# Kernel tuning notes

Hardware: AMD Instinct MI355X
Metric: run time of the kernel (lower is better)

## Reference

```python
import jax, jax.numpy as jnp
import numpy as np

S = 192          # spatial_size
N = 100000       # active input sites
CIN, M, M2, NCLS = 3, 32, 64, 50
EPS = 1e-4       # scn BatchNorm eps
OFFS = np.array([[dx, dy, dz] for dx in (-1, 0, 1) for dy in (-1, 0, 1) for dz in (-1, 0, 1)], dtype=np.int64)


def _build_nbr(coords, size):
    # coords: [n,3] unique int64. Returns [n,27] int32 neighbor index (-1 = inactive site),
    # i.e. the submanifold-convolution rulebook built via sorted-key hashing.
    n = coords.shape[0]
    keys = (coords[:, 0] * size + coords[:, 1]) * size + coords[:, 2]
    order = np.argsort(keys)
    sk = keys[order]
    nbr = np.full((n, 27), -1, dtype=np.int32)
    for k, off in enumerate(OFFS):
        nc = coords + off
        ok = np.all((nc >= 0) & (nc < size), axis=1)
        qk = (nc[:, 0] * size + nc[:, 1]) * size + nc[:, 2]
        pos = np.searchsorted(sk, qk).clip(0, n - 1)
        hit = ok & (sk[pos] == qk)
        nbr[hit, k] = order[pos[hit]].astype(np.int32)
    return nbr


def setup_inputs() -> dict:
    rng = np.random.default_rng(0)
    raw = rng.integers(0, S, size=(130000, 3), dtype=np.int64)
    keys = (raw[:, 0] * S + raw[:, 1]) * S + raw[:, 2]
    _, first = np.unique(keys, return_index=True)
    coords = raw[np.sort(first)][:N]          # N unique active voxels
    nbr_fine = _build_nbr(coords, S)
    # stride-2 / filter-2 downsample rulebook: coarse sites = unique(coords // 2)
    S2 = S // 2
    cc = coords // 2
    ckeys = (cc[:, 0] * S2 + cc[:, 1]) * S2 + cc[:, 2]
    uk, parent = np.unique(ckeys, return_inverse=True)
    ccoords = np.column_stack((uk // (S2 * S2), (uk // S2) % S2, uk % S2))
    nbr_coarse = _build_nbr(ccoords, S2)
    offset_id = (coords[:, 0] % 2) * 4 + (coords[:, 1] % 2) * 2 + coords[:, 2] % 2
    key = jax.random.key(0)
    ks = jax.random.split(key, 8)
    def w(k, shape, fan):
        return jax.random.normal(k, shape, jnp.float32) * (1.0 / np.sqrt(fan))
    return dict(
        coords=jnp.asarray(coords, jnp.int32),
        features=jax.random.normal(ks[0], (N, CIN), jnp.float32),
        nbr_fine=jnp.asarray(nbr_fine),
        nbr_coarse=jnp.asarray(nbr_coarse),
        parent=jnp.asarray(parent.astype(np.int32)),
        offset_id=jnp.asarray(offset_id.astype(np.int32)),
        num_coarse=int(uk.shape[0]),
        w_in=w(ks[1], (27, CIN, M), 27 * CIN),
        w_b1=w(ks[2], (27, M, M), 27 * M),
        w_down=w(ks[3], (8, M, M2), 8 * M),
        w_b2=w(ks[4], (27, M2, M2), 27 * M2),
        w_up=w(ks[5], (8, M2, M), 8 * M2),
        w_b3=w(ks[6], (27, 2 * M, M), 27 * 2 * M),
        g1=jnp.ones((M,)), b1=jnp.zeros((M,)),
        gd=jnp.ones((M,)), bd=jnp.zeros((M,)),
        g2=jnp.ones((M2,)), b2=jnp.zeros((M2,)),
        gu=jnp.ones((M2,)), bu=jnp.zeros((M2,)),
        g3=jnp.ones((2 * M,)), b3=jnp.zeros((2 * M,)),
        go=jnp.ones((M,)), bo=jnp.zeros((M,)),
        w_lin=w(ks[7], (M, NCLS), M),
        b_lin=jnp.zeros((NCLS,)),
    )


def _subm_conv(f, nbr, W):
    # f: [n,Cin], nbr: [n,27] (-1 = inactive), W: [27,Cin,Cout]
    mask = nbr >= 0
    g = f[jnp.where(mask, nbr, 0)] * mask[..., None]  # [n,27,Cin]
    return jnp.einsum('nkc,kcd->nd', g, W)


def _bnrelu(f, gamma, beta):
    mu = f.mean(0)
    var = ((f - mu) ** 2).mean(0)
    return jax.nn.relu((f - mu) * (gamma / jnp.sqrt(var + EPS)) + beta)


def _down(f, parent, off_id, W, nc):
    # strided 2^3 conv: out[parent] += W[offset(child)] @ f[child]
    out = jnp.zeros((nc, W.shape[2]), f.dtype)
    for o in range(8):
        sel = (off_id == o)[:, None].astype(f.dtype)
        out = out + jax.ops.segment_sum((f * sel) @ W[o], parent, num_segments=nc)
    return out


def _up(g, parent, off_id, W):
    # 2^3 deconv back to fine sites
    gp = g[parent]
    out = jnp.zeros((gp.shape[0], W.shape[2]), g.dtype)
    for o in range(8):
        out = out + (off_id == o)[:, None].astype(g.dtype) * (gp @ W[o])
    return out


def reference(coords, features, nbr_fine, nbr_coarse, parent, offset_id, num_coarse,
              w_in, w_b1, w_down, w_b2, w_up, w_b3,
              g1, b1, gd, bd, g2, b2, gu, bu, g3, b3, go, bo, w_lin, b_lin):
    # InputLayer (coords unique -> identity) + SubmanifoldConvolution(CIN->M)
    f = _subm_conv(features, nbr_fine, w_in)
    # UNet level 0 block (pre-activation)
    f = _subm_conv(_bnrelu(f, g1, b1), nbr_fine, w_b1)
    skip = f
    # downsample: BNReLU + Convolution(M->M2, 2, 2)
    g = _down(_bnrelu(f, gd, bd), parent, offset_id, w_down, num_coarse)
    # UNet level 1 block
    g = _subm_conv(_bnrelu(g, g2, b2), nbr_coarse, w_b2)
    # upsample: BNReLU + Deconvolution(M2->M, 2, 2)
    u = _up(_bnrelu(g, gu, bu), parent, offset_id, w_up)
    # JoinTable + block (2M -> M)
    f = jnp.concatenate([skip, u], axis=1)
    f = _subm_conv(_bnrelu(f, g3, b3), nbr_fine, w_b3)
    # top-level BatchNormReLU(M) + OutputLayer + Linear head
    f = _bnrelu(f, go, bo)
    return f @ w_lin + b_lin
```

## Files before the change

### kernel.cpp

```cpp
#include <hip/hip_runtime.h>

#define EPS_BN 1e-4f
constexpr int BLK = 256;
constexpr int ECAPF = 256;
constexpr int ECAPC = 640;

__global__ __launch_bounds__(64) void build_subm_k(
    const int* __restrict__ nbr, int n, int ecap,
    int* __restrict__ seg, int* __restrict__ ent) {
  int T = blockIdx.x, r = threadIdx.x;
  int i = T * 64 + r;
  bool valid = i < n;
  int base = 0;
  if (r == 0) seg[T * 28] = 0;
#pragma unroll 1
  for (int k = 0; k < 27; ++k) {
    int j = valid ? nbr[(size_t)i * 27 + k] : -1;
    bool act = j >= 0;
    unsigned long long mb = __ballot(act);
    int pre = __popcll(mb & ((1ull << r) - 1));
    if (act && base + pre < ecap)
      ent[(size_t)T * ecap + base + pre] = (r << 25) | j;
    base += __popcll(mb);
    if (r == 0) seg[T * 28 + k + 1] = base;
  }
}

__global__ __launch_bounds__(BLK) void child_scatter_k(
    const int* __restrict__ parent, const int* __restrict__ offid, int n,
    int* __restrict__ ccnt, int* __restrict__ cent) {
  int i = blockIdx.x * BLK + threadIdx.x;
  if (i >= n) return;
  int p = parent[i];
  int slot = atomicAdd(&ccnt[p], 1);
  cent[p * 8 + slot] = i | (offid[i] << 25);
}

__global__ __launch_bounds__(64) void build_down_k(
    const int* __restrict__ ccnt, const int* __restrict__ cent, int nc,
    int* __restrict__ segd, int* __restrict__ entd) {
  int T = blockIdx.x, r = threadIdx.x;
  int p = T * 64 + r;
  bool valid = p < nc;
  int cn = valid ? ccnt[p] : 0;
  int e[8];
#pragma unroll
  for (int s = 0; s < 8; ++s) e[s] = s < cn ? cent[p * 8 + s] : -1;
  int base = 0;
  if (r == 0) segd[T * 9] = 0;
#pragma unroll 1
  for (int oo = 0; oo < 8; ++oo) {
#pragma unroll
    for (int s = 0; s < 8; ++s) {
      bool act = e[s] >= 0 && (e[s] >> 25) == oo;
      unsigned long long mb = __ballot(act);
      int pre = __popcll(mb & ((1ull << r) - 1));
      if (act) entd[(size_t)T * 512 + base + pre] = (r << 25) | (e[s] & 0x1FFFFFF);
      base += __popcll(mb);
    }
    if (r == 0) segd[T * 9 + oo + 1] = base;
  }
}

__global__ __launch_bounds__(64) void build_up_k(
    const int* __restrict__ parent, const int* __restrict__ offid, int n,
    int* __restrict__ segu, int* __restrict__ entu) {
  int T = blockIdx.x, r = threadIdx.x;
  int i = T * 64 + r;
  bool valid = i < n;
  int o = valid ? offid[i] : -1;
  int pa = valid ? parent[i] : 0;
  int base = 0;
  if (r == 0) segu[T * 9] = 0;
#pragma unroll 1
  for (int oo = 0; oo < 8; ++oo) {
    bool act = o == oo;
    unsigned long long mb = __ballot(act);
    int pre = __popcll(mb & ((1ull << r) - 1));
    if (act) entu[(size_t)T * 64 + base + pre] = (r << 25) | pa;
    base += __popcll(mb);
    if (r == 0) segu[T * 9 + oo + 1] = base;
  }
}

template <int CI, int CO, int KT, bool BN, bool CAT>
__global__ __launch_bounds__(BLK) void tconv_k(
    const float* __restrict__ inA, const float* __restrict__ inB,
    const int* __restrict__ seg, const int* __restrict__ ent, int ecap,
    const float* __restrict__ stA, const float* __restrict__ stB,
    const float* __restrict__ W, float* __restrict__ out, int n) {
  constexpr int GO = CO / 16;
  constexpr int XP = CI + 4;
  constexpr int AP = CO + 4;
  __shared__ float lw[CI * CO];
  __shared__ float lx[64 * XP];
  __shared__ float lacc[64 * AP];
  int t = threadIdx.x;
  int T = blockIdx.x;
  const int* segT = seg + T * (KT + 1);
  const int* entT = ent + (size_t)T * ecap;

  for (int idx = t; idx < 64 * AP; idx += BLK) lacc[idx] = 0.f;

#pragma unroll 1
  for (int k = 0; k < KT; ++k) {
    int e0 = segT[k], e1 = segT[k + 1];
    int m = e1 - e0;
    if (m == 0) continue;
    const float4* wsrc = reinterpret_cast<const float4*>(W + (size_t)k * CI * CO);
    for (int idx = t; idx < CI * CO / 4; idx += BLK)
      reinterpret_cast<float4*>(lw)[idx] = wsrc[idx];
    for (int idx = t; idx < m * (CI / 4); idx += BLK) {
      int p = idx / (CI / 4), c4 = idx - p * (CI / 4);
      int j = entT[e0 + p] & 0x1FFFFFF;
      int cb = c4 * 4;
      float4 x;
      const float* st;
      int cc;
      if constexpr (CAT) {
        if (cb < CI / 2) { x = *reinterpret_cast<const float4*>(inA + (size_t)j * (CI / 2) + cb); st = stA; cc = cb; }
        else             { x = *reinterpret_cast<const float4*>(inB + (size_t)j * (CI / 2) + cb - CI / 2); st = stB; cc = cb - CI / 2; }
      } else {
        x = *reinterpret_cast<const float4*>(inA + (size_t)j * CI + cb); st = stA; cc = cb;
      }
      float v[4] = {x.x, x.y, x.z, x.w};
      if constexpr (BN) {
        constexpr int SH = CAT ? CI / 2 : CI;
#pragma unroll
        for (int q = 0; q < 4; ++q) {
          float y = fmaf(v[q], st[cc + q], st[SH + cc + q]);
          v[q] = y > 0.f ? y : 0.f;
        }
      }
      *reinterpret_cast<float4*>(&lx[p * XP + cb]) = make_float4(v[0], v[1], v[2], v[3]);
    }
    __syncthreads();
    int s = t >> 4, g = (t & 15) * GO;
#pragma unroll 1
    for (int p0 = 0; p0 < m; p0 += 16) {
      int p = p0 + s;
      if (p < m) {
        int r = entT[e0 + p] >> 25;
        float acc[GO];
#pragma unroll
        for (int b = 0; b < GO; ++b) acc[b] = 0.f;
#pragma unroll
        for (int c4 = 0; c4 < CI / 4; ++c4) {
          float4 xq = *reinterpret_cast<const float4*>(&lx[p * XP + c4 * 4]);
          float xs[4] = {xq.x, xq.y, xq.z, xq.w};
#pragma unroll
          for (int q = 0; q < 4; ++q) {
            const float* wr = &lw[(c4 * 4 + q) * CO + g];
            if constexpr (GO == 4) {
              float4 wv = *reinterpret_cast<const float4*>(wr);
              acc[0] = fmaf(xs[q], wv.x, acc[0]);
              acc[1] = fmaf(xs[q], wv.y, acc[1]);
              acc[2] = fmaf(xs[q], wv.z, acc[2]);
              acc[3] = fmaf(xs[q], wv.w, acc[3]);
            } else {
              float2 wv = *reinterpret_cast<const float2*>(wr);
              acc[0] = fmaf(xs[q], wv.x, acc[0]);
              acc[1] = fmaf(xs[q], wv.y, acc[1]);
            }
          }
        }
        float* ap = &lacc[r * AP + g];
        if constexpr (GO == 4) {
          float4 old = *reinterpret_cast<float4*>(ap);
          *reinterpret_cast<float4*>(ap) =
              make_float4(old.x + acc[0], old.y + acc[1], old.z + acc[2], old.w + acc[3]);
        } else {
          float2 old = *reinterpret_cast<float2*>(ap);
          *reinterpret_cast<float2*>(ap) = make_float2(old.x + acc[0], old.y + acc[1]);
        }
      }
    }
    __syncthreads();
  }
  __syncthreads();
  for (int idx = t; idx < 64 * (CO / 4); idx += BLK) {
    int r = idx / (CO / 4), c4 = idx - r * (CO / 4);
    int row = T * 64 + r;
    if (row < n)
      *reinterpret_cast<float4*>(out + (size_t)row * CO + c4 * 4) =
          *reinterpret_cast<const float4*>(&lacc[r * AP + c4 * 4]);
  }
}

__global__ __launch_bounds__(BLK) void conv_in_k(
    const float* __restrict__ feat, const int* __restrict__ nbr,
    const float* __restrict__ W, float* __restrict__ out, int n) {
  int i = blockIdx.x * BLK + threadIdx.x;
  if (i >= n) return;
  float acc[32];
#pragma unroll
  for (int c = 0; c < 32; ++c) acc[c] = 0.f;
  const int* nr = nbr + (size_t)i * 27;
#pragma unroll 1
  for (int k = 0; k < 27; ++k) {
    int j = nr[k];
    if (j < 0) continue;
    float x0 = feat[j * 3 + 0], x1 = feat[j * 3 + 1], x2 = feat[j * 3 + 2];
    const float* w0 = W + k * 96;
#pragma unroll
    for (int co = 0; co < 8; ++co) {
      float4 a = *reinterpret_cast<const float4*>(w0 + co * 4);
      float4 b = *reinterpret_cast<const float4*>(w0 + 32 + co * 4);
      float4 cc = *reinterpret_cast<const float4*>(w0 + 64 + co * 4);
      acc[4*co+0] = fmaf(x0, a.x, fmaf(x1, b.x, fmaf(x2, cc.x, acc[4*co+0])));
      acc[4*co+1] = fmaf(x0, a.y, fmaf(x1, b.y, fmaf(x2, cc.y, acc[4*co+1])));
      acc[4*co+2] = fmaf(x0, a.z, fmaf(x1, b.z, fmaf(x2, cc.z, acc[4*co+2])));
      acc[4*co+3] = fmaf(x0, a.w, fmaf(x1, b.w, fmaf(x2, cc.w, acc[4*co+3])));
    }
  }
  float* o = out + (size_t)i * 32;
#pragma unroll
  for (int co = 0; co < 8; ++co)
    *reinterpret_cast<float4*>(o + co * 4) = make_float4(acc[4*co], acc[4*co+1], acc[4*co+2], acc[4*co+3]);
}

template <int C>
__global__ __launch_bounds__(BLK) void stats_k(
    const float* __restrict__ f, int n, float* __restrict__ sums) {
  constexpr int G = BLK / C;
  int c = threadIdx.x % C;
  int g = threadIdx.x / C;
  float s = 0.f, ss = 0.f;
  for (int r = blockIdx.x * G + g; r < n; r += gridDim.x * G) {
    float x = f[(size_t)r * C + c];
    s += x;
    ss += x * x;
  }
  __shared__ float ls[BLK], lss[BLK];
  ls[threadIdx.x] = s;
  lss[threadIdx.x] = ss;
  __syncthreads();
  if (threadIdx.x < C) {
    float ts = 0.f, tss = 0.f;
#pragma unroll
    for (int q = 0; q < G; ++q) { ts += ls[q * C + c]; tss += lss[q * C + c]; }
    atomicAdd(&sums[c], ts);
    atomicAdd(&sums[C + c], tss);
  }
}

__global__ void finalize_k(const float* __restrict__ sums,
                           const float* __restrict__ gamma,
                           const float* __restrict__ beta, float inv_n,
                           float* __restrict__ st, int C) {
  int c = threadIdx.x;
  if (c >= C) return;
  float mu = sums[c] * inv_n;
  float var = sums[C + c] * inv_n - mu * mu;
  float sc = gamma[c] / sqrtf(var + EPS_BN);
  st[c] = sc;
  st[C + c] = beta[c] - mu * sc;
}

__global__ __launch_bounds__(BLK) void head_k(
    const float* __restrict__ fin, const float* __restrict__ st,
    const float* __restrict__ Wl, const float* __restrict__ bl,
    float* __restrict__ out, int n) {
  __shared__ float lw[32 * 50];
  __shared__ float lb[52];
  for (int idx = threadIdx.x; idx < 1600; idx += BLK) lw[idx] = Wl[idx];
  if (threadIdx.x < 50) lb[threadIdx.x] = bl[threadIdx.x];
  __syncthreads();
  int i = blockIdx.x * BLK + threadIdx.x;
  if (i >= n) return;
  float x[32];
  const float* fj = fin + (size_t)i * 32;
#pragma unroll
  for (int c4 = 0; c4 < 8; ++c4) {
    float4 v = *reinterpret_cast<const float4*>(fj + c4 * 4);
    float vs[4] = {v.x, v.y, v.z, v.w};
#pragma unroll
    for (int q = 0; q < 4; ++q) {
      int c = c4 * 4 + q;
      float y = fmaf(vs[q], st[c], st[32 + c]);
      x[c] = y > 0.f ? y : 0.f;
    }
  }
  float acc[50];
#pragma unroll
  for (int co = 0; co < 50; ++co) acc[co] = lb[co];
#pragma unroll 4
  for (int c = 0; c < 32; ++c) {
#pragma unroll
    for (int co = 0; co < 50; ++co) acc[co] = fmaf(x[c], lw[c * 50 + co], acc[co]);
  }
  float* o = out + (size_t)i * 50;
#pragma unroll
  for (int co = 0; co < 25; ++co)
    *reinterpret_cast<float2*>(o + co * 2) = make_float2(acc[co * 2], acc[co * 2 + 1]);
}

extern "C" void kernel_launch(void* const* d_in, const int* in_sizes, int n_in,
                              void* d_out, int out_size, void* d_ws, size_t ws_size,
                              hipStream_t stream) {
  const float* feat   = (const float*)d_in[1];
  const int*   nbrF   = (const int*)d_in[2];
  const int*   nbrC   = (const int*)d_in[3];
  const int*   parent = (const int*)d_in[4];
  const int*   offid  = (const int*)d_in[5];
  const float* w_in   = (const float*)d_in[7];
  const float* w_b1   = (const float*)d_in[8];
  const float* w_down = (const float*)d_in[9];
  const float* w_b2   = (const float*)d_in[10];
  const float* w_up   = (const float*)d_in[11];
  const float* w_b3   = (const float*)d_in[12];
  const float* g1 = (const float*)d_in[13], *b1 = (const float*)d_in[14];
  const float* gd = (const float*)d_in[15], *bd = (const float*)d_in[16];
  const float* g2 = (const float*)d_in[17], *b2 = (const float*)d_in[18];
  const float* gu = (const float*)d_in[19], *bu = (const float*)d_in[20];
  const float* g3 = (const float*)d_in[21], *b3 = (const float*)d_in[22];
  const float* go = (const float*)d_in[23], *bo = (const float*)d_in[24];
  const float* w_lin = (const float*)d_in[25];
  const float* b_lin = (const float*)d_in[26];
  float* out = (float*)d_out;

  int N  = in_sizes[4];
  int NC = in_sizes[3] / 27;
  int ntF = (N + 63) / 64, ntC = (NC + 63) / 64;

  size_t szF = (size_t)N * 32;
  size_t szG = (size_t)NC * 64;
  size_t SA = szG > szF ? szG : szF;

  float* ws  = (float*)d_ws;
  float* A   = ws;
  float* f2  = A + SA;
  float* gCu = f2 + szF;
  float* sums1 = gCu + szG;
  float* sumsD = sums1 + 64;
  float* sums2 = sumsD + 64;
  float* sumsU = sums2 + 128;
  float* sums4 = sumsU + 128;
  float* sums5 = sums4 + 64;
  float* st1  = sums5 + 64;
  float* stD  = st1 + 64;
  float* st3a = stD + 64;
  float* st2  = st3a + 64;
  float* stU  = st2 + 128;
  float* st3b = stU + 128;
  float* stO  = st3b + 64;
  int* segF = (int*)(stO + 64);
  int* entF = segF + (size_t)ntF * 28;
  int* segC = entF + (size_t)ntF * ECAPF;
  int* entC = segC + (size_t)ntC * 28;
  int* ccnt = entC + (size_t)ntC * ECAPC;
  int* cent = ccnt + NC;
  int* segD = cent + (size_t)NC * 8;
  int* entD = segD + (size_t)ntC * 9;
  int* segU = entD + (size_t)ntC * 512;
  int* entU = segU + (size_t)ntF * 9;

  hipMemsetAsync(sums1, 0, 512 * sizeof(float), stream);
  hipMemsetAsync(ccnt, 0, (size_t)NC * sizeof(int), stream);

  int gridN = (N + BLK - 1) / BLK;
  int sgrid = 304;
  float invN = 1.f / (float)N, invC = 1.f / (float)NC;

  build_subm_k<<<ntF, 64, 0, stream>>>(nbrF, N, ECAPF, segF, entF);
  build_subm_k<<<ntC, 64, 0, stream>>>(nbrC, NC, ECAPC, segC, entC);
  child_scatter_k<<<gridN, BLK, 0, stream>>>(parent, offid, N, ccnt, cent);
  build_down_k<<<ntC, 64, 0, stream>>>(ccnt, cent, NC, segD, entD);
  build_up_k<<<ntF, 64, 0, stream>>>(parent, offid, N, segU, entU);

  conv_in_k<<<gridN, BLK, 0, stream>>>(feat, nbrF, w_in, A, N);
  stats_k<32><<<sgrid, BLK, 0, stream>>>(A, N, sums1);
  finalize_k<<<1, 64, 0, stream>>>(sums1, g1, b1, invN, st1, 32);

  tconv_k<32, 32, 27, true, false><<<ntF, BLK, 0, stream>>>(
      A, nullptr, segF, entF, ECAPF, st1, nullptr, w_b1, f2, N);
  stats_k<32><<<sgrid, BLK, 0, stream>>>(f2, N, sumsD);
  finalize_k<<<1, 64, 0, stream>>>(sumsD, gd, bd, invN, stD, 32);
  finalize_k<<<1, 64, 0, stream>>>(sumsD, g3, b3, invN, st3a, 32);

  tconv_k<32, 64, 8, true, false><<<ntC, BLK, 0, stream>>>(
      f2, nullptr, segD, entD, 512, stD, nullptr, w_down, gCu, NC);
  stats_k<64><<<sgrid, BLK, 0, stream>>>(gCu, NC, sums2);
  finalize_k<<<1, 64, 0, stream>>>(sums2, g2, b2, invC, st2, 64);

  tconv_k<64, 64, 27, true, false><<<ntC, BLK, 0, stream>>>(
      gCu, nullptr, segC, entC, ECAPC, st2, nullptr, w_b2, A, NC);
  stats_k<64><<<sgrid, BLK, 0, stream>>>(A, NC, sumsU);
  finalize_k<<<1, 64, 0, stream>>>(sumsU, gu, bu, invC, stU, 64);

  tconv_k<64, 32, 8, true, false><<<ntF, BLK, 0, stream>>>(
      A, nullptr, segU, entU, 64, stU, nullptr, w_up, gCu, N);
  stats_k<32><<<sgrid, BLK, 0, stream>>>(gCu, N, sums4);
  finalize_k<<<1, 64, 0, stream>>>(sums4, g3 + 32, b3 + 32, invN, st3b, 32);

  tconv_k<64, 32, 27, true, true><<<ntF, BLK, 0, stream>>>(
      f2, gCu, segF, entF, ECAPF, st3a, st3b, w_b3, A, N);
  stats_k<32><<<sgrid, BLK, 0, stream>>>(A, N, sums5);
  finalize_k<<<1, 64, 0, stream>>>(sums5, go, bo, invN, stO, 32);

  head_k<<<gridN, BLK, 0, stream>>>(A, stO, w_lin, b_lin, out, N);
}
```

Measured before the change: 566.8 us.

## Fuse BN stats into convs, double-buffer weights, drop LDS gather staging

BatchNorm statistics are now accumulated inside each convolution epilogue with atomics, and the finalize step is folded into the consumer kernel's prologue. This removes the separate stats and finalize launches and their extra passes over the feature maps. The tconv kernel drops the shared-memory gather buffer and reads neighbor features straight from global memory, applying BN+ReLU per element. It also double-buffers per-offset weights through registers and skips empty offsets. The fine and upsample rulebook builders are merged and the entry caps raised, trading more global gathers per output group and atomic contention for fewer launches and syncs.

```diff
diff --git a/kernel.cpp b/kernel.cpp
--- a/kernel.cpp
+++ b/kernel.cpp
@@ -2,12 +2,14 @@
 
 #define EPS_BN 1e-4f
 constexpr int BLK = 256;
-constexpr int ECAPF = 256;
-constexpr int ECAPC = 640;
-
-__global__ __launch_bounds__(64) void build_subm_k(
-    const int* __restrict__ nbr, int n, int ecap,
-    int* __restrict__ seg, int* __restrict__ ent) {
+constexpr int ECAPF = 512;
+constexpr int ECAPC = 1024;
+
+__global__ __launch_bounds__(64) void build_fine_k(
+    const int* __restrict__ nbr, const int* __restrict__ parent,
+    const int* __restrict__ offid, int n, int ecap,
+    int* __restrict__ seg, int* __restrict__ ent,
+    int* __restrict__ segu, int* __restrict__ entu) {
   int T = blockIdx.x, r = threadIdx.x;
   int i = T * 64 + r;
   bool valid = i < n;
@@ -24,6 +26,40 @@
     base += __popcll(mb);
     if (r == 0) seg[T * 28 + k + 1] = base;
   }
+  int o = valid ? offid[i] : -1;
+  int pa = valid ? parent[i] : 0;
+  base = 0;
+  if (r == 0) segu[T * 9] = 0;
+#pragma unroll 1
+  for (int oo = 0; oo < 8; ++oo) {
+    bool act = o == oo;
+    unsigned long long mb = __ballot(act);
+    int pre = __popcll(mb & ((1ull << r) - 1));
+    if (act) entu[(size_t)T * 64 + base + pre] = (r << 25) | pa;
+    base += __popcll(mb);
+    if (r == 0) segu[T * 9 + oo + 1] = base;
+  }
+}
+
+__global__ __launch_bounds__(64) void build_subm_k(
+    const int* __restrict__ nbr, int n, int ecap,
+    int* __restrict__ seg, int* __restrict__ ent) {
+  int T = blockIdx.x, r = threadIdx.x;
+  int i = T * 64 + r;
+  bool valid = i < n;
+  int base = 0;
+  if (r == 0) seg[T * 28] = 0;
+#pragma unroll 1
+  for (int k = 0; k < 27; ++k) {
+    int j = valid ? nbr[(size_t)i * 27 + k] : -1;
+    bool act = j >= 0;
+    unsigned long long mb = __ballot(act);
+    int pre = __popcll(mb & ((1ull << r) - 1));
+    if (act && base + pre < ecap)
+      ent[(size_t)T * ecap + base + pre] = (r << 25) | j;
+    base += __popcll(mb);
+    if (r == 0) seg[T * 28 + k + 1] = base;
+  }
 }
 
 __global__ __launch_bounds__(BLK) void child_scatter_k(
@@ -62,122 +98,148 @@
   }
 }
 
-__global__ __launch_bounds__(64) void build_up_k(
-    const int* __restrict__ parent, const int* __restrict__ offid, int n,
-    int* __restrict__ segu, int* __restrict__ entu) {
-  int T = blockIdx.x, r = threadIdx.x;
-  int i = T * 64 + r;
-  bool valid = i < n;
-  int o = valid ? offid[i] : -1;
-  int pa = valid ? parent[i] : 0;
-  int base = 0;
-  if (r == 0) segu[T * 9] = 0;
-#pragma unroll 1
-  for (int oo = 0; oo < 8; ++oo) {
-    bool act = o == oo;
-    unsigned long long mb = __ballot(act);
-    int pre = __popcll(mb & ((1ull << r) - 1));
-    if (act) entu[(size_t)T * 64 + base + pre] = (r << 25) | pa;
-    base += __popcll(mb);
-    if (r == 0) segu[T * 9 + oo + 1] = base;
-  }
-}
-
-template <int CI, int CO, int KT, bool BN, bool CAT>
+template <int CI, int CO, int KT, bool CAT>
 __global__ __launch_bounds__(BLK) void tconv_k(
     const float* __restrict__ inA, const float* __restrict__ inB,
     const int* __restrict__ seg, const int* __restrict__ ent, int ecap,
-    const float* __restrict__ stA, const float* __restrict__ stB,
-    const float* __restrict__ W, float* __restrict__ out, int n) {
+    const float* __restrict__ sumsA, const float* __restrict__ gA,
+    const float* __restrict__ bA, float invA,
+    const float* __restrict__ sumsB, const float* __restrict__ gB,
+    const float* __restrict__ bB, float invB,
+    const float* __restrict__ W, float* __restrict__ out, int n,
+    float* __restrict__ osums) {
   constexpr int GO = CO / 16;
-  constexpr int XP = CI + 4;
   constexpr int AP = CO + 4;
-  __shared__ float lw[CI * CO];
-  __shared__ float lx[64 * XP];
+  constexpr int WSZ = CI * CO;
+  constexpr int WL = WSZ / 4 / BLK;
+  __shared__ float lw[2][WSZ];
   __shared__ float lacc[64 * AP];
+  __shared__ float lst[2 * CI];
   int t = threadIdx.x;
   int T = blockIdx.x;
+
+  if constexpr (CAT) {
+    if (t < CI / 2) {
+      float mu = sumsA[t] * invA, var = sumsA[CI / 2 + t] * invA - mu * mu;
+      float sc = gA[t] / sqrtf(var + EPS_BN);
+      lst[t] = sc; lst[CI + t] = bA[t] - mu * sc;
+    } else if (t < CI) {
+      int c = t - CI / 2;
+      float mu = sumsB[c] * invB, var = sumsB[CI / 2 + c] * invB - mu * mu;
+      float sc = gB[c] / sqrtf(var + EPS_BN);
+      lst[t] = sc; lst[CI + t] = bB[c] - mu * sc;
+    }
+  } else {
+    if (t < CI) {
+      float mu = sumsA[t] * invA, var = sumsA[CI + t] * invA - mu * mu;
+      float sc = gA[t] / sqrtf(var + EPS_BN);
+      lst[t] = sc; lst[CI + t] = bA[t] - mu * sc;
+    }
+  }
+  for (int idx = t; idx < 64 * AP; idx += BLK) lacc[idx] = 0.f;
+
   const int* segT = seg + T * (KT + 1);
   const int* entT = ent + (size_t)T * ecap;
 
-  for (int idx = t; idx < 64 * AP; idx += BLK) lacc[idx] = 0.f;
-
-#pragma unroll 1
-  for (int k = 0; k < KT; ++k) {
-    int e0 = segT[k], e1 = segT[k + 1];
-    int m = e1 - e0;
-    if (m == 0) continue;
-    const float4* wsrc = reinterpret_cast<const float4*>(W + (size_t)k * CI * CO);
-    for (int idx = t; idx < CI * CO / 4; idx += BLK)
-      reinterpret_cast<float4*>(lw)[idx] = wsrc[idx];
-    for (int idx = t; idx < m * (CI / 4); idx += BLK) {
-      int p = idx / (CI / 4), c4 = idx - p * (CI / 4);
-      int j = entT[e0 + p] & 0x1FFFFFF;
-      int cb = c4 * 4;
-      float4 x;
-      const float* st;
-      int cc;
-      if constexpr (CAT) {
-        if (cb < CI / 2) { x = *reinterpret_cast<const float4*>(inA + (size_t)j * (CI / 2) + cb); st = stA; cc = cb; }
-        else             { x = *reinterpret_cast<const float4*>(inB + (size_t)j * (CI / 2) + cb - CI / 2); st = stB; cc = cb - CI / 2; }
-      } else {
-        x = *reinterpret_cast<const float4*>(inA + (size_t)j * CI + cb); st = stA; cc = cb;
+  int k = KT, e0 = 0, e1 = 0;
+  {
+    int prev = segT[0];
+#pragma unroll 1
+    for (int q = 0; q < KT; ++q) {
+      int cur = segT[q + 1];
+      if (cur > prev) { k = q; e0 = prev; e1 = cur; break; }
+      prev = cur;
+    }
+  }
+  if (k < KT) {
+    const float4* wsrc = reinterpret_cast<const float4*>(W + (size_t)k * WSZ);
+#pragma unroll
+    for (int q = 0; q < WL; ++q)
+      reinterpret_cast<float4*>(lw[0])[t + q * BLK] = wsrc[t + q * BLK];
+  }
+  __syncthreads();
+
+  int par = 0;
+#pragma unroll 1
+  while (k < KT) {
+    int kn = KT, f0 = 0, f1 = 0;
+    {
+      int prev = e1;
+#pragma unroll 1
+      for (int q = k + 1; q < KT; ++q) {
+        int cur = segT[q + 1];
+        if (cur > prev) { kn = q; f0 = prev; f1 = cur; break; }
+        prev = cur;
       }
-      float v[4] = {x.x, x.y, x.z, x.w};
-      if constexpr (BN) {
-        constexpr int SH = CAT ? CI / 2 : CI;
-#pragma unroll
-        for (int q = 0; q < 4; ++q) {
-          float y = fmaf(v[q], st[cc + q], st[SH + cc + q]);
-          v[q] = y > 0.f ? y : 0.f;
-        }
-      }
-      *reinterpret_cast<float4*>(&lx[p * XP + cb]) = make_float4(v[0], v[1], v[2], v[3]);
-    }
-    __syncthreads();
+    }
+    float4 wreg[WL];
+    if (kn < KT) {
+      const float4* wsrc = reinterpret_cast<const float4*>(W + (size_t)kn * WSZ);
+#pragma unroll
+      for (int q = 0; q < WL; ++q) wreg[q] = wsrc[t + q * BLK];
+    }
+    int ee0 = min(e0, ecap), ee1 = min(e1, ecap);
+    int m = ee1 - ee0;
     int s = t >> 4, g = (t & 15) * GO;
+    const float* wp = lw[par];
 #pragma unroll 1
     for (int p0 = 0; p0 < m; p0 += 16) {
       int p = p0 + s;
       if (p < m) {
-        int r = entT[e0 + p] >> 25;
+        int e = entT[ee0 + p];
+        int r = e >> 25, j = e & 0x1FFFFFF;
         float acc[GO];
 #pragma unroll
         for (int b = 0; b < GO; ++b) acc[b] = 0.f;
 #pragma unroll
         for (int c4 = 0; c4 < CI / 4; ++c4) {
-          float4 xq = *reinterpret_cast<const float4*>(&lx[p * XP + c4 * 4]);
-          float xs[4] = {xq.x, xq.y, xq.z, xq.w};
+          int cb = c4 * 4;
+          float4 x;
+          if constexpr (CAT) {
+            if (cb < CI / 2) x = *reinterpret_cast<const float4*>(inA + (size_t)j * (CI / 2) + cb);
+            else             x = *reinterpret_cast<const float4*>(inB + (size_t)j * (CI / 2) + (cb - CI / 2));
+          } else {
+            x = *reinterpret_cast<const float4*>(inA + (size_t)j * CI + cb);
+          }
+          float xs[4] = {x.x, x.y, x.z, x.w};
 #pragma unroll
           for (int q = 0; q < 4; ++q) {
-            const float* wr = &lw[(c4 * 4 + q) * CO + g];
+            float y = fmaf(xs[q], lst[cb + q], lst[CI + cb + q]);
+            y = y > 0.f ? y : 0.f;
+            const float* wr = wp + (cb + q) * CO + g;
             if constexpr (GO == 4) {
               float4 wv = *reinterpret_cast<const float4*>(wr);
-              acc[0] = fmaf(xs[q], wv.x, acc[0]);
-              acc[1] = fmaf(xs[q], wv.y, acc[1]);
-              acc[2] = fmaf(xs[q], wv.z, acc[2]);
-              acc[3] = fmaf(xs[q], wv.w, acc[3]);
+              acc[0] = fmaf(y, wv.x, acc[0]);
+              acc[1] = fmaf(y, wv.y, acc[1]);
+              acc[2] = fmaf(y, wv.z, acc[2]);
+              acc[3] = fmaf(y, wv.w, acc[3]);
             } else {
               float2 wv = *reinterpret_cast<const float2*>(wr);
-              acc[0] = fmaf(xs[q], wv.x, acc[0]);
-              acc[1] = fmaf(xs[q], wv.y, acc[1]);
+              acc[0] = fmaf(y, wv.x, acc[0]);
+              acc[1] = fmaf(y, wv.y, acc[1]);
             }
           }
         }
         float* ap = &lacc[r * AP + g];
         if constexpr (GO == 4) {
-          float4 old = *reinterpret_cast<float4*>(ap);
+          float4 o = *reinterpret_cast<float4*>(ap);
           *reinterpret_cast<float4*>(ap) =
-              make_float4(old.x + acc[0], old.y + acc[1], old.z + acc[2], old.w + acc[3]);
+              make_float4(o.x + acc[0], o.y + acc[1], o.z + acc[2], o.w + acc[3]);
         } else {
-          float2 old = *reinterpret_cast<float2*>(ap);
-          *reinterpret_cast<float2*>(ap) = make_float2(old.x + acc[0], old.y + acc[1]);
+          float2 o = *reinterpret_cast<float2*>(ap);
+          *reinterpret_cast<float2*>(ap) = make_float2(o.x + acc[0], o.y + acc[1]);
         }
       }
     }
+    if (kn < KT) {
+#pragma unroll
+      for (int q = 0; q < WL; ++q)
+        reinterpret_cast<float4*>(lw[par ^ 1])[t + q * BLK] = wreg[q];
+    }
     __syncthreads();
-  }
-  __syncthreads();
+    par ^= 1; k = kn; e0 = f0; e1 = f1;
+  }
+
   for (int idx = t; idx < 64 * (CO / 4); idx += BLK) {
     int r = idx / (CO / 4), c4 = idx - r * (CO / 4);
     int row = T * 64 + r;
@@ -185,20 +247,30 @@
       *reinterpret_cast<float4*>(out + (size_t)row * CO + c4 * 4) =
           *reinterpret_cast<const float4*>(&lacc[r * AP + c4 * 4]);
   }
+  if (t < CO) {
+    float s = 0.f, ss = 0.f;
+#pragma unroll 4
+    for (int r = 0; r < 64; ++r) {
+      float x = lacc[r * AP + t];
+      s += x; ss = fmaf(x, x, ss);
+    }
+    atomicAdd(&osums[t], s);
+    atomicAdd(&osums[CO + t], ss);
+  }
 }
 
 __global__ __launch_bounds__(BLK) void conv_in_k(
     const float* __restrict__ feat, const int* __restrict__ nbr,
-    const float* __restrict__ W, float* __restrict__ out, int n) {
+    const float* __restrict__ W, float* __restrict__ out, int n,
+    float* __restrict__ osums) {
   int i = blockIdx.x * BLK + threadIdx.x;
-  if (i >= n) return;
+  bool valid = i < n;
   float acc[32];
 #pragma unroll
   for (int c = 0; c < 32; ++c) acc[c] = 0.f;
-  const int* nr = nbr + (size_t)i * 27;
 #pragma unroll 1
   for (int k = 0; k < 27; ++k) {
-    int j = nr[k];
+    int j = valid ? nbr[(size_t)i * 27 + k] : -1;
     if (j < 0) continue;
     float x0 = feat[j * 3 + 0], x1 = feat[j * 3 + 1], x2 = feat[j * 3 + 2];
     const float* w0 = W + k * 96;
@@ -213,60 +285,50 @@
       acc[4*co+3] = fmaf(x0, a.w, fmaf(x1, b.w, fmaf(x2, cc.w, acc[4*co+3])));
     }
   }
-  float* o = out + (size_t)i * 32;
-#pragma unroll
-  for (int co = 0; co < 8; ++co)
-    *reinterpret_cast<float4*>(o + co * 4) = make_float4(acc[4*co], acc[4*co+1], acc[4*co+2], acc[4*co+3]);
-}
-
-template <int C>
-__global__ __launch_bounds__(BLK) void stats_k(
-    const float* __restrict__ f, int n, float* __restrict__ sums) {
-  constexpr int G = BLK / C;
-  int c = threadIdx.x % C;
-  int g = threadIdx.x / C;
-  float s = 0.f, ss = 0.f;
-  for (int r = blockIdx.x * G + g; r < n; r += gridDim.x * G) {
-    float x = f[(size_t)r * C + c];
-    s += x;
-    ss += x * x;
-  }
-  __shared__ float ls[BLK], lss[BLK];
-  ls[threadIdx.x] = s;
-  lss[threadIdx.x] = ss;
+  if (valid) {
+    float* o = out + (size_t)i * 32;
+#pragma unroll
+    for (int co = 0; co < 8; ++co)
+      *reinterpret_cast<float4*>(o + co * 4) = make_float4(acc[4*co], acc[4*co+1], acc[4*co+2], acc[4*co+3]);
+  }
+  __shared__ float red[2][4][32];
+  int w = threadIdx.x >> 6;
+#pragma unroll
+  for (int c = 0; c < 32; ++c) {
+    float v = acc[c], q = acc[c] * acc[c];
+#pragma unroll
+    for (int off = 32; off; off >>= 1) {
+      v += __shfl_down(v, off);
+      q += __shfl_down(q, off);
+    }
+    if ((threadIdx.x & 63) == 0) { red[0][w][c] = v; red[1][w][c] = q; }
+  }
   __syncthreads();
-  if (threadIdx.x < C) {
-    float ts = 0.f, tss = 0.f;
-#pragma unroll
-    for (int q = 0; q < G; ++q) { ts += ls[q * C + c]; tss += lss[q * C + c]; }
-    atomicAdd(&sums[c], ts);
-    atomicAdd(&sums[C + c], tss);
-  }
-}
-
-__global__ void finalize_k(const float* __restrict__ sums,
-                           const float* __restrict__ gamma,
-                           const float* __restrict__ beta, float inv_n,
-                           float* __restrict__ st, int C) {
-  int c = threadIdx.x;
-  if (c >= C) return;
-  float mu = sums[c] * inv_n;
-  float var = sums[C + c] * inv_n - mu * mu;
-  float sc = gamma[c] / sqrtf(var + EPS_BN);
-  st[c] = sc;
-  st[C + c] = beta[c] - mu * sc;
+  if (threadIdx.x < 64) {
+    int kind = threadIdx.x >> 5, c = threadIdx.x & 31;
+    float s = red[kind][0][c] + red[kind][1][c] + red[kind][2][c] + red[kind][3][c];
+    atomicAdd(&osums[kind * 32 + c], s);
+  }
 }
 
 __global__ __launch_bounds__(BLK) void head_k(
-    const float* __restrict__ fin, const float* __restrict__ st,
+    const float* __restrict__ fin, const float* __restrict__ sums,
+    const float* __restrict__ gm, const float* __restrict__ bt, float inv_n,
     const float* __restrict__ Wl, const float* __restrict__ bl,
     float* __restrict__ out, int n) {
   __shared__ float lw[32 * 50];
   __shared__ float lb[52];
-  for (int idx = threadIdx.x; idx < 1600; idx += BLK) lw[idx] = Wl[idx];
-  if (threadIdx.x < 50) lb[threadIdx.x] = bl[threadIdx.x];
+  __shared__ float lst[64];
+  int t = threadIdx.x;
+  if (t < 32) {
+    float mu = sums[t] * inv_n, var = sums[32 + t] * inv_n - mu * mu;
+    float sc = gm[t] / sqrtf(var + EPS_BN);
+    lst[t] = sc; lst[32 + t] = bt[t] - mu * sc;
+  }
+  for (int idx = t; idx < 1600; idx += BLK) lw[idx] = Wl[idx];
+  if (t < 50) lb[t] = bl[t];
   __syncthreads();
-  int i = blockIdx.x * BLK + threadIdx.x;
+  int i = blockIdx.x * BLK + t;
   if (i >= n) return;
   float x[32];
   const float* fj = fin + (size_t)i * 32;
@@ -277,7 +339,7 @@
 #pragma unroll
     for (int q = 0; q < 4; ++q) {
       int c = c4 * 4 + q;
-      float y = fmaf(vs[q], st[c], st[32 + c]);
+      float y = fmaf(vs[q], lst[c], lst[32 + c]);
       x[c] = y > 0.f ? y : 0.f;
     }
   }
@@ -309,12 +371,12 @@
   const float* w_b2   = (const float*)d_in[10];
   const float* w_up   = (const float*)d_in[11];
   const float* w_b3   = (const float*)d_in[12];
-  const float* g1 = (const float*)d_in[13], *b1 = (const float*)d_in[14];
-  const float* gd = (const float*)d_in[15], *bd = (const float*)d_in[16];
-  const float* g2 = (const float*)d_in[17], *b2 = (const float*)d_in[18];
-  const float* gu = (const float*)d_in[19], *bu = (const float*)d_in[20];
-  const float* g3 = (const float*)d_in[21], *b3 = (const float*)d_in[22];
-  const float* go = (const float*)d_in[23], *bo = (const float*)d_in[24];
+  const float* g1v = (const float*)d_in[13], *b1v = (const float*)d_in[14];
+  const float* gdv = (const float*)d_in[15], *bdv = (const float*)d_in[16];
+  const float* g2v = (const float*)d_in[17], *b2v = (const float*)d_in[18];
+  const float* guv = (const float*)d_in[19], *buv = (const float*)d_in[20];
+  const float* g3v = (const float*)d_in[21], *b3v = (const float*)d_in[22];
+  const float* gov = (const float*)d_in[23], *bov = (const float*)d_in[24];
   const float* w_lin = (const float*)d_in[25];
   const float* b_lin = (const float*)d_in[26];
   float* out = (float*)d_out;
@@ -331,72 +393,59 @@
   float* A   = ws;
   float* f2  = A + SA;
   float* gCu = f2 + szF;
-  float* sums1 = gCu + szG;
+  float* sums1 = gCu + SA;
   float* sumsD = sums1 + 64;
   float* sums2 = sumsD + 64;
   float* sumsU = sums2 + 128;
   float* sums4 = sumsU + 128;
   float* sums5 = sums4 + 64;
-  float* st1  = sums5 + 64;
-  float* stD  = st1 + 64;
-  float* st3a = stD + 64;
-  float* st2  = st3a + 64;
-  float* stU  = st2 + 128;
-  float* st3b = stU + 128;
-  float* stO  = st3b + 64;
-  int* segF = (int*)(stO + 64);
+  int* ccnt = (int*)(sums5 + 64);
+  int* cent = ccnt + NC;
+  int* segF = cent + (size_t)NC * 8;
   int* entF = segF + (size_t)ntF * 28;
   int* segC = entF + (size_t)ntF * ECAPF;
   int* entC = segC + (size_t)ntC * 28;
-  int* ccnt = entC + (size_t)ntC * ECAPC;
-  int* cent = ccnt + NC;
-  int* segD = cent + (size_t)NC * 8;
+  int* segD = entC + (size_t)ntC * ECAPC;
   int* entD = segD + (size_t)ntC * 9;
   int* segU = entD + (size_t)ntC * 512;
   int* entU = segU + (size_t)ntF * 9;
 
-  hipMemsetAsync(sums1, 0, 512 * sizeof(float), stream);
-  hipMemsetAsync(ccnt, 0, (size_t)NC * sizeof(int), stream);
+  hipMemsetAsync(sums1, 0, (512 + NC) * sizeof(float), stream);
 
   int gridN = (N + BLK - 1) / BLK;
-  int sgrid = 304;
   float invN = 1.f / (float)N, invC = 1.f / (float)NC;
 
-  build_subm_k<<<ntF, 64, 0, stream>>>(nbrF, N, ECAPF, segF, entF);
+  build_fine_k<<<ntF, 64, 0, stream>>>(nbrF, parent, offid, N, ECAPF, segF, entF, segU, entU);
   build_subm_k<<<ntC, 64, 0, stream>>>(nbrC, NC, ECAPC, segC, entC);
   child_scatter_k<<<gridN, BLK, 0, stream>>>(parent, offid, N, ccnt, cent);
   build_down_k<<<ntC, 64, 0, stream>>>(ccnt, cent, NC, segD, entD);
-  build_up_k<<<ntF, 64, 0, stream>>>(parent, offid, N, segU, entU);
-
-  conv_in_k<<<gridN, BLK, 0, stream>>>(feat, nbrF, w_in, A, N);
-  stats_k<32><<<sgrid, BLK, 0, stream>>>(A, N, sums1);
-  finalize_k<<<1, 64, 0, stream>>>(sums1, g1, b1, invN, st1, 32);
-
-  tconv_k<32, 32, 27, true, false><<<ntF, BLK, 0, stream>>>(
-      A, nullptr, segF, entF, ECAPF, st1, nullptr, w_b1, f2, N);
-  stats_k<32><<<sgrid, BLK, 0, stream>>>(f2, N, sumsD);
-  finalize_k<<<1, 64, 0, stream>>>(sumsD, gd, bd, invN, stD, 32);
-  finalize_k<<<1, 64, 0, stream>>>(sumsD, g3, b3, invN, st3a, 32);
-
-  tconv_k<32, 64, 8, true, false><<<ntC, BLK, 0, stream>>>(
-      f2, nullptr, segD, entD, 512, stD, nullptr, w_down, gCu, NC);
-  stats_k<64><<<sgrid, BLK, 0, stream>>>(gCu, NC, sums2);
-  finalize_k<<<1, 64, 0, stream>>>(sums2, g2, b2, invC, st2, 64);
-
-  tconv_k<64, 64, 27, true, false><<<ntC, BLK, 0, stream>>>(
-      gCu, nullptr, segC, entC, ECAPC, st2, nullptr, w_b2, A, NC);
-  stats_k<64><<<sgrid, BLK, 0, stream>>>(A, NC, sumsU);
-  finalize_k<<<1, 64, 0, stream>>>(sumsU, gu, bu, invC, stU, 64);
-
-  tconv_k<64, 32, 8, true, false><<<ntF, BLK, 0, stream>>>(
-      A, nullptr, segU, entU, 64, stU, nullptr, w_up, gCu, N);
-  stats_k<32><<<sgrid, BLK, 0, stream>>>(gCu, N, sums4);
-  finalize_k<<<1, 64, 0, stream>>>(sums4, g3 + 32, b3 + 32, invN, st3b, 32);
-
-  tconv_k<64, 32, 27, true, true><<<ntF, BLK, 0, stream>>>(
-      f2, gCu, segF, entF, ECAPF, st3a, st3b, w_b3, A, N);
-  stats_k<32><<<sgrid, BLK, 0, stream>>>(A, N, sums5);
-  finalize_k<<<1, 64, 0, stream>>>(sums5, go, bo, invN, stO, 32);
-
-  head_k<<<gridN, BLK, 0, stream>>>(A, stO, w_lin, b_lin, out, N);
-}
+
+  conv_in_k<<<gridN, BLK, 0, stream>>>(feat, nbrF, w_in, A, N, sums1);
+
+  tconv_k<32, 32, 27, false><<<ntF, BLK, 0, stream>>>(
+      A, nullptr, segF, entF, ECAPF,
+      sums1, g1v, b1v, invN, nullptr, nullptr, nullptr, 0.f,
+      w_b1, f2, N, sumsD);
+
+  tconv_k<32, 64, 8, false><<<ntC, BLK, 0, stream>>>(
+      f2, nullptr, segD, entD, 512,
+      sumsD, gdv, bdv, invN, nullptr, nullptr, nullptr, 0.f,
+      w_down, gCu, NC, sums2);
+
+  tconv_k<64, 64, 27, false><<<ntC, BLK, 0, stream>>>(
+      gCu, nullptr, segC, entC, ECAPC,
+      sums2, g2v, b2v, invC, nullptr, nullptr, nullptr, 0.f,
+      w_b2, A, NC, sumsU);
+
+  tconv_k<64, 32, 8, false><<<ntF, BLK, 0, stream>>>(
+      A, nullptr, segU, entU, 64,
+      sumsU, guv, buv, invC, nullptr, nullptr, nullptr, 0.f,
+      w_up, gCu, N, sums4);
+
+  tconv_k<64, 32, 27, true><<<ntF, BLK, 0, stream>>>(
+      f2, gCu, segF, entF, ECAPF,
+      sumsD, g3v, b3v, invN, sums4, g3v + 32, b3v + 32, invN,
+      w_b3, A, N, sums5);
+
+  head_k<<<gridN, BLK, 0, stream>>>(A, sums5, gov, bov, invN, w_lin, b_lin, out, N);
+}
```

After: 1.054 ms. 1.86x slower.
